# Performance work log

Hardware: AMD Instinct MI355X
Metric: run time of the kernel (lower is better)

## Reference

```python
import jax, jax.numpy as jnp
import numpy as np

B, N, IN_C, HEAD_C, H, EXPAND, OUT_C = 4, 2048, 256, 32, 8, 1024, 256
QKV_DIM = HEAD_C * H * 2 + IN_C * H  # 2560
LN_EPS = 1e-5


def setup_inputs() -> dict:
    key = jax.random.key(0)
    ks = jax.random.split(key, 6)
    s = lambda fan: 1.0 / np.sqrt(fan)
    return {
        "x": jax.random.normal(ks[0], (B, N, IN_C), jnp.float32),
        "ln1_g": jnp.ones((IN_C,), jnp.float32),
        "ln1_b": jnp.zeros((IN_C,), jnp.float32),
        "Wqkv": jax.random.normal(ks[1], (IN_C, QKV_DIM), jnp.float32) * s(IN_C),
        "bqkv": jnp.zeros((QKV_DIM,), jnp.float32),
        "Wm": jax.random.normal(ks[2], (IN_C * H, IN_C), jnp.float32) * s(IN_C * H),
        "bm": jnp.zeros((IN_C,), jnp.float32),
        "ln2_g": jnp.ones((IN_C,), jnp.float32),
        "ln2_b": jnp.zeros((IN_C,), jnp.float32),
        "W1": jax.random.normal(ks[3], (IN_C, EXPAND), jnp.float32) * s(IN_C),
        "b1": jnp.zeros((EXPAND,), jnp.float32),
        "W2": jax.random.normal(ks[4], (EXPAND, OUT_C), jnp.float32) * s(EXPAND),
        "b2": jnp.zeros((OUT_C,), jnp.float32),
    }


def _ln(x, g, b):
    m = x.mean(-1, keepdims=True)
    v = jnp.mean(jnp.square(x - m), axis=-1, keepdims=True)
    return (x - m) * jax.lax.rsqrt(v + LN_EPS) * g + b


def reference(x, ln1_g, ln1_b, Wqkv, bqkv, Wm, bm, ln2_g, ln2_b, W1, b1, W2, b2):
    scale = HEAD_C ** -0.5
    qkv = _ln(x, ln1_g, ln1_b) @ Wqkv + bqkv  # [B,N,QKV_DIM]
    q, k, v = jnp.split(qkv, [HEAD_C * H, 2 * HEAD_C * H], axis=-1)
    q = q.reshape(B, N, H, HEAD_C)  # H-major channel split, matches einops
    k = k.reshape(B, N, H, HEAD_C)
    v = v.reshape(B, N, H, IN_C)    # NOTE: V has in_c channels per head
    attn = jax.nn.softmax(jnp.einsum('bnhc,bmhc->bhnm', q, k) * scale, axis=-1)
    out = jnp.einsum('bhnm,bmhc->bnhc', attn, v).reshape(B, N, H * IN_C)
    x = x + out @ Wm + bm  # residual + merge-head projection
    h = jax.nn.gelu(_ln(x, ln2_g, ln2_b) @ W1 + b1, approximate=False)
    return (h @ W2 + b2) + x  # shortcut is Identity (in_c == out_c)
```

## Files before the change

### kernel.cpp

```cpp
#include <hip/hip_runtime.h>

typedef unsigned short u16;
typedef __attribute__((ext_vector_type(8))) short bf8_t;
typedef __attribute__((ext_vector_type(4))) float f4_t;
typedef __attribute__((ext_vector_type(16))) float fx16;

__device__ __forceinline__ float bf2f(u16 v) {
    union { unsigned u; float f; } c; c.u = ((unsigned)v) << 16; return c.f;
}
__device__ __forceinline__ u16 f2bf(float f) {
    union { float f; unsigned u; } c; c.f = f;
    unsigned r = 0x7FFFu + ((c.u >> 16) & 1u);
    return (u16)((c.u + r) >> 16);
}

#define B_   4
#define N_   2048
#define INC  256
#define H_   8
#define ROWS 8192

#define SEG_X     0
#define SEG_LN1G  2097152
#define SEG_LN1B  2097408
#define SEG_WQKV  2097664
#define SEG_BQKV  2753024
#define SEG_WM    2755584
#define SEG_BM    3279872
#define SEG_LN2G  3280128
#define SEG_LN2B  3280384
#define SEG_W1    3280640
#define SEG_B1    3542784
#define SEG_W2    3543808
#define SEG_B2    3805952
#define SEG_TOT   3806208

__global__ __launch_bounds__(256) void conv_k(
    const void* p0, const void* p1, const void* p2, const void* p3, const void* p4,
    const void* p5, const void* p6, const void* p7, const void* p8, const void* p9,
    const void* p10, const void* p11, const void* p12,
    u16* __restrict__ dst, u16* __restrict__ y, int* __restrict__ mkz)
{
    const int t = threadIdx.x;
    const int blk = blockIdx.x;

    __shared__ int sflag;
    if (t == 0) sflag = 0;
    __syncthreads();
    int bad = 0;
    #pragma unroll
    for (int k2 = 0; k2 < 4; ++k2) {
        float v = bf2f(((const u16*)p0)[t * 4 + k2]);
        if (!(fabsf(v) < 1e10f)) bad = 1;
    }
    if (bad) atomicOr(&sflag, 1);
    __syncthreads();
    const int flag = sflag;

    if (blk == 8192 && t < 32) mkz[t] = 0;

    const int i = blk * 256 + t;
    if (i >= SEG_TOT) return;

    if (i < SEG_LN1G) {
        float v = flag ? ((const float*)p0)[i] : bf2f(((const u16*)p0)[i]);
        dst[i] = f2bf(v);
        float s = v, s2 = v * v;
        #pragma unroll
        for (int d = 1; d < 64; d <<= 1) {
            s  += __shfl_xor(s,  d, 64);
            s2 += __shfl_xor(s2, d, 64);
        }
        __shared__ float rs[8];
        int w = t >> 6;
        if ((t & 63) == 0) { rs[w] = s; rs[4 + w] = s2; }
        __syncthreads();
        s  = rs[0] + rs[1] + rs[2] + rs[3];
        s2 = rs[4] + rs[5] + rs[6] + rs[7];
        float mean = s * (1.0f / INC);
        float var  = s2 * (1.0f / INC) - mean * mean;
        float inv  = rsqrtf(var + 1e-5f);
        float g  = flag ? ((const float*)p1)[t] : bf2f(((const u16*)p1)[t]);
        float bb = flag ? ((const float*)p2)[t] : bf2f(((const u16*)p2)[t]);
        y[i] = f2bf((v - mean) * inv * g + bb);
        return;
    }

    const void* p; int j;
    if      (i < SEG_LN1B) { p = p1;  j = i - SEG_LN1G; }
    else if (i < SEG_WQKV) { p = p2;  j = i - SEG_LN1B; }
    else if (i < SEG_BQKV) { p = p3;  int ii = i - SEG_WQKV;
                             int n = ii >> 8, k = ii & 255; j = k * 2560 + n; }
    else if (i < SEG_WM)   { p = p4;  j = i - SEG_BQKV; }
    else if (i < SEG_BM)   { p = p5;  int ii = i - SEG_WM;
                             int n = ii >> 11, k = ii & 2047; j = k * 256 + n; }
    else if (i < SEG_LN2G) { p = p6;  j = i - SEG_BM; }
    else if (i < SEG_LN2B) { p = p7;  j = i - SEG_LN2G; }
    else if (i < SEG_W1)   { p = p8;  j = i - SEG_LN2B; }
    else if (i < SEG_B1)   { p = p9;  int ii = i - SEG_W1;
                             int n = ii >> 8, k = ii & 255; j = k * 1024 + n; }
    else if (i < SEG_W2)   { p = p10; j = i - SEG_B1; }
    else if (i < SEG_B2)   { p = p11; int ii = i - SEG_W2;
                             int n = ii >> 10, k = ii & 1023; j = k * 256 + n; }
    else                   { p = p12; j = i - SEG_B2; }
    dst[i] = flag ? f2bf(((const float*)p)[j]) : ((const u16*)p)[j];
}

template<bool BF16IN>
__global__ __launch_bounds__(256) void ln_k(const void* __restrict__ xp,
        const u16* __restrict__ g, const u16* __restrict__ b, u16* __restrict__ y)
{
    int row  = blockIdx.x * 4 + (threadIdx.x >> 6);
    int lane = threadIdx.x & 63;
    int c0   = lane * 4;
    float v[4];
    if (BF16IN) {
        ushort4 u = *(const ushort4*)((const u16*)xp + (size_t)row * INC + c0);
        v[0] = bf2f(u.x); v[1] = bf2f(u.y); v[2] = bf2f(u.z); v[3] = bf2f(u.w);
    } else {
        float4 f = *(const float4*)((const float*)xp + (size_t)row * INC + c0);
        v[0] = f.x; v[1] = f.y; v[2] = f.z; v[3] = f.w;
    }
    float s = v[0] + v[1] + v[2] + v[3];
    float s2 = v[0]*v[0] + v[1]*v[1] + v[2]*v[2] + v[3]*v[3];
    #pragma unroll
    for (int d = 1; d < 64; d <<= 1) {
        s  += __shfl_xor(s,  d, 64);
        s2 += __shfl_xor(s2, d, 64);
    }
    float mean = s * (1.0f / INC);
    float var  = s2 * (1.0f / INC) - mean * mean;
    float inv  = rsqrtf(var + 1e-5f);
    ushort4 gv = *(const ushort4*)(g + c0);
    ushort4 bv = *(const ushort4*)(b + c0);
    ushort4 o;
    o.x = f2bf((v[0] - mean) * inv * bf2f(gv.x) + bf2f(bv.x));
    o.y = f2bf((v[1] - mean) * inv * bf2f(gv.y) + bf2f(bv.y));
    o.z = f2bf((v[2] - mean) * inv * bf2f(gv.z) + bf2f(bv.z));
    o.w = f2bf((v[3] - mean) * inv * bf2f(gv.w) + bf2f(bv.w));
    *(ushort4*)(y + (size_t)row * INC + c0) = o;
}

enum { EP_QKV = 0, EP_MERGE = 1, EP_GELU = 2, EP_FFN2 = 3 };

template<int MODE>
__global__ __launch_bounds__(256) void gemm_big(
    const u16* __restrict__ A, const u16* __restrict__ Bt,
    const u16* __restrict__ bias, void* __restrict__ outp,
    u16* __restrict__ qh, u16* __restrict__ kh, u16* __restrict__ vh,
    int* __restrict__ mkz, int N, int K)
{
    const int t = threadIdx.x;
    const int w = t >> 6, lane = t & 63;
    const int l15 = lane & 15, quad = lane >> 4;
    const int col0 = blockIdx.x * 64;
    const int row0 = blockIdx.y * 256;
    const int mrow = row0 + w * 64;

    const u16* Ap = A  + (size_t)(mrow + l15) * K + quad * 8;
    const u16* Bp = Bt + (size_t)(col0 + l15) * K + quad * 8;

    f4_t acc[4][4];
    #pragma unroll
    for (int mi = 0; mi < 4; ++mi)
        #pragma unroll
        for (int ni = 0; ni < 4; ++ni)
            acc[mi][ni] = (f4_t){0.f, 0.f, 0.f, 0.f};

    for (int k0 = 0; k0 < K; k0 += 32) {
        bf8_t a[4], bb[4];
        #pragma unroll
        for (int mi = 0; mi < 4; ++mi)
            a[mi] = *(const bf8_t*)(Ap + (size_t)mi * 16 * K + k0);
        #pragma unroll
        for (int ni = 0; ni < 4; ++ni)
            bb[ni] = *(const bf8_t*)(Bp + (size_t)ni * 16 * K + k0);
        #pragma unroll
        for (int ni = 0; ni < 4; ++ni)
            #pragma unroll
            for (int mi = 0; mi < 4; ++mi)
                acc[mi][ni] = __builtin_amdgcn_mfma_f32_16x16x32_bf16(
                    a[mi], bb[ni], acc[mi][ni], 0, 0, 0);
    }

    if (MODE == EP_QKV) {
        if (col0 >= 512) {
            __shared__ u16 Ts[64][268];
            #pragma unroll
            for (int mi = 0; mi < 4; ++mi)
                #pragma unroll
                for (int ni = 0; ni < 4; ++ni) {
                    float bz = bf2f(bias[col0 + ni * 16 + l15]);
                    #pragma unroll
                    for (int r = 0; r < 4; ++r)
                        Ts[ni * 16 + l15][w * 64 + mi * 16 + quad * 4 + r] =
                            f2bf(acc[mi][ni][r] + bz);
                }
            __syncthreads();
            int vcg = col0 - 512;
            int hh  = vcg >> 8;
            int bb2 = row0 >> 11, nb = row0 & 2047;
            int bhh = bb2 * 8 + hh;
            int tok4 = t & 3, cl = (t >> 2) & 63;
            int vc = (vcg & 255) + cl;
            #pragma unroll
            for (int kb = 0; kb < 16; ++kb) {
                u16* dp = vh + (((size_t)bhh * 128 + ((nb >> 4) + kb)) * 256 + vc) * 16 + tok4 * 4;
                *(ushort4*)dp = *(const ushort4*)&Ts[cl][kb * 16 + tok4 * 4];
            }
        } else if (col0 < 256) {
            #pragma unroll
            for (int mi = 0; mi < 4; ++mi)
                #pragma unroll
                for (int r = 0; r < 4; ++r) {
                    int rg = mrow + mi * 16 + quad * 4 + r;
                    int bb2 = rg >> 11, n = rg & 2047;
                    #pragma unroll
                    for (int ni = 0; ni < 4; ++ni) {
                        int col = col0 + ni * 16 + l15;
                        float v = acc[mi][ni][r] + bf2f(bias[col]);
                        qh[(((size_t)(bb2 * 8 + (col >> 5))) * 2048 + n) * 32 + (col & 31)] = f2bf(v);
                    }
                }
        } else {
            const int hA  = (col0 - 256) >> 5;
            const int bb2 = row0 >> 11;
            float mxA = 0.f, mxB = 0.f;
            #pragma unroll
            for (int mi = 0; mi < 4; ++mi)
                #pragma unroll
                for (int r = 0; r < 4; ++r) {
                    int rg = mrow + mi * 16 + quad * 4 + r;
                    int n = rg & 2047;
                    float vv[4];
                    #pragma unroll
                    for (int ni = 0; ni < 4; ++ni) {
                        int col = col0 + ni * 16 + l15;
                        float v = acc[mi][ni][r] + bf2f(bias[col]);
                        vv[ni] = v;
                        int c2 = col - 256;
                        int hd = c2 >> 5, ch = c2 & 31;
                        kh[(((size_t)(bb2 * 8 + hd) * 64 + (n >> 5)) * 2 + (ch >> 4)) * 512
                           + (n & 31) * 16 + (ch & 15)] = f2bf(v);
                    }
                    float sA = vv[0] * vv[0] + vv[1] * vv[1];
                    float sB = vv[2] * vv[2] + vv[3] * vv[3];
                    #pragma unroll
                    for (int d = 1; d < 16; d <<= 1) {
                        sA += __shfl_xor(sA, d, 64);
                        sB += __shfl_xor(sB, d, 64);
                    }
                    mxA = fmaxf(mxA, sA);
                    mxB = fmaxf(mxB, sB);
                }
            if ((lane & 15) == 0) {
                atomicMax(mkz + bb2 * 8 + hA,     __float_as_int(mxA));
                atomicMax(mkz + bb2 * 8 + hA + 1, __float_as_int(mxB));
            }
        }
    } else {
        float bz[4];
        #pragma unroll
        for (int ni = 0; ni < 4; ++ni) bz[ni] = bf2f(bias[col0 + ni * 16 + l15]);
        #pragma unroll
        for (int mi = 0; mi < 4; ++mi)
            #pragma unroll
            for (int r = 0; r < 4; ++r) {
                int rg = mrow + mi * 16 + quad * 4 + r;
                size_t base = (size_t)rg * N + col0 + l15;
                #pragma unroll
                for (int ni = 0; ni < 4; ++ni) {
                    float v = acc[mi][ni][r] + bz[ni];
                    v = 0.5f * v * (1.0f + erff(v * 0.70710678118654752f));
                    ((u16*)outp)[base + ni * 16] = f2bf(v);
                }
            }
    }
}

template<int MODE>
__global__ __launch_bounds__(256) void gemm_mfma(
    const u16* __restrict__ A, const u16* __restrict__ Bt,
    const u16* __restrict__ bias, const void* __restrict__ res,
    void* __restrict__ outp, int N, int K)
{
    const int t = threadIdx.x;
    const int w = t >> 6, lane = t & 63;
    const int l15 = lane & 15, quad = lane >> 4;
    const int col0 = blockIdx.x * 64;
    const int row0 = blockIdx.y * 128;
    const int mrow = row0 + w * 32;

    const u16* Ap = A  + (size_t)(mrow + l15) * K + quad * 8;
    const u16* Bp = Bt + (size_t)(col0 + l15) * K + quad * 8;

    f4_t acc[2][4];
    #pragma unroll
    for (int mi = 0; mi < 2; ++mi)
        #pragma unroll
        for (int ni = 0; ni < 4; ++ni)
            acc[mi][ni] = (f4_t){0.f, 0.f, 0.f, 0.f};

    for (int k0 = 0; k0 < K; k0 += 64) {
        bf8_t a[2][2], bb[4][2];
        #pragma unroll
        for (int kc = 0; kc < 2; ++kc) {
            #pragma unroll
            for (int mi = 0; mi < 2; ++mi)
                a[mi][kc] = *(const bf8_t*)(Ap + (size_t)mi * 16 * K + k0 + kc * 32);
            #pragma unroll
            for (int ni = 0; ni < 4; ++ni)
                bb[ni][kc] = *(const bf8_t*)(Bp + (size_t)ni * 16 * K + k0 + kc * 32);
        }
        #pragma unroll
        for (int kc = 0; kc < 2; ++kc)
            #pragma unroll
            for (int ni = 0; ni < 4; ++ni)
                #pragma unroll
                for (int mi = 0; mi < 2; ++mi)
                    acc[mi][ni] = __builtin_amdgcn_mfma_f32_16x16x32_bf16(
                        a[mi][kc], bb[ni][kc], acc[mi][ni], 0, 0, 0);
    }

    float bz[4];
    #pragma unroll
    for (int ni = 0; ni < 4; ++ni) bz[ni] = bf2f(bias[col0 + ni * 16 + l15]);
    #pragma unroll
    for (int mi = 0; mi < 2; ++mi)
        #pragma unroll
        for (int r = 0; r < 4; ++r) {
            int rg = mrow + mi * 16 + quad * 4 + r;
            size_t base = (size_t)rg * N + col0 + l15;
            if (MODE == EP_MERGE) {
                const u16* R = (const u16*)res;
                #pragma unroll
                for (int ni = 0; ni < 4; ++ni)
                    ((float*)outp)[base + ni * 16] =
                        acc[mi][ni][r] + bz[ni] + bf2f(R[base + ni * 16]);
            } else {
                const float* R = (const float*)res;
                #pragma unroll
                for (int ni = 0; ni < 4; ++ni)
                    ((float*)outp)[base + ni * 16] =
                        acc[mi][ni][r] + bz[ni] + R[base + ni * 16];
            }
        }
}

__global__ __launch_bounds__(256) void attn_k(
    const u16* __restrict__ qh, const u16* __restrict__ kh,
    const u16* __restrict__ vhT, const float* __restrict__ mk2,
    u16* __restrict__ ao)
{
    const int t = threadIdx.x;
    const int w = t >> 6, lane = t & 63;
    const int l31 = lane & 31, hi = lane >> 5;
    const int id = blockIdx.x;
    const int qt = (id >> 3) & 31;
    const int bh = (id >> 8) * 8 + (id & 7);
    const int b  = bh >> 3, h = bh & 7;
    const int n0 = qt * 64;
    const float SCALE = 0.17677669529663687f;
    const int sw = (l31 & 7) << 4;

    __shared__ __align__(16) u16 Pb[2][64][128];
    __shared__ float lds_l[4][64];
    __shared__ float lds_t[64];

    bf8_t qf[2][2];
    #pragma unroll
    for (int m = 0; m < 2; ++m)
        #pragma unroll
        for (int ks = 0; ks < 2; ++ks)
            qf[m][ks] = *(const bf8_t*)(qh + ((size_t)bh * 2048 + n0 + m * 32 + l31) * 32
                                        + ks * 16 + hi * 8);

    float mrow[2];
    #pragma unroll
    for (int m = 0; m < 2; ++m) {
        float q2 = 0.f;
        #pragma unroll
        for (int ks = 0; ks < 2; ++ks)
            #pragma unroll
            for (int i = 0; i < 8; ++i) {
                float qv = bf2f((u16)qf[m][ks][i]); q2 += qv * qv;
            }
        q2 += __shfl_xor(q2, 32, 64);
        mrow[m] = SCALE * sqrtf(q2 * mk2[bh]);
    }

    fx16 acc[2][2];
    #pragma unroll
    for (int a1 = 0; a1 < 2; ++a1)
        #pragma unroll
        for (int a2 = 0; a2 < 2; ++a2)
            #pragma unroll
            for (int e = 0; e < 16; ++e) acc[a1][a2][e] = 0.f;
    float lsum[2] = {0.f, 0.f};

    fx16 z16;
    #pragma unroll
    for (int e = 0; e < 16; ++e) z16[e] = 0.f;

    auto finish = [&](const fx16& s, int m, int g, char* base) {
        float p0 = __expf(fmaf(s[4 * g + 0], SCALE, -mrow[m]));
        float p1 = __expf(fmaf(s[4 * g + 1], SCALE, -mrow[m]));
        float p2 = __expf(fmaf(s[4 * g + 2], SCALE, -mrow[m]));
        float p3 = __expf(fmaf(s[4 * g + 3], SCALE, -mrow[m]));
        lsum[m] += (p0 + p1) + (p2 + p3);
        ushort4 pk;
        pk.x = f2bf(p0); pk.y = f2bf(p1); pk.z = f2bf(p2); pk.w = f2bf(p3);
        *(ushort4*)(base + (m * 32 + l31) * 256 + ((w * 64 + 16 * g + 8 * hi) ^ sw)) = pk;
    };

    bf8_t kA0, kA1;
    auto ldK = [&](int c) {
        const u16* kp = kh + ((size_t)bh * 64 + c * 4 + w) * 1024 + l31 * 16 + hi * 8;
        kA0 = *(const bf8_t*)kp;
        kA1 = *(const bf8_t*)(kp + 512);
    };

    {
        ldK(0);
        fx16 sA = __builtin_amdgcn_mfma_f32_32x32x16_bf16(kA0, qf[0][0], z16, 0, 0, 0);
        sA = __builtin_amdgcn_mfma_f32_32x32x16_bf16(kA1, qf[0][1], sA, 0, 0, 0);
        fx16 sB = __builtin_amdgcn_mfma_f32_32x32x16_bf16(kA0, qf[1][0], z16, 0, 0, 0);
        sB = __builtin_amdgcn_mfma_f32_32x32x16_bf16(kA1, qf[1][1], sB, 0, 0, 0);
        ldK(1);
        char* base0 = (char*)&Pb[0][0][0];
        #pragma unroll
        for (int g = 0; g < 4; ++g) finish(sA, 0, g, base0);
        #pragma unroll
        for (int g = 0; g < 4; ++g) finish(sB, 1, g, base0);
    }

    const u16* vpb = vhT + (((size_t)bh * 128) * 256 + w * 64 + l31) * 16 + hi * 8;
    bf8_t vb0 = *(const bf8_t*)vpb;
    bf8_t vb1 = *(const bf8_t*)(vpb + 512);

    int buf = 0;
    for (int c = 0; c < 16; ++c, buf ^= 1) {
        __syncthreads();
        const bool qn = (c < 15);
        fx16 sA, sB;
        if (qn) {
            sA = __builtin_amdgcn_mfma_f32_32x32x16_bf16(kA0, qf[0][0], z16, 0, 0, 0);
            sA = __builtin_amdgcn_mfma_f32_32x32x16_bf16(kA1, qf[0][1], sA, 0, 0, 0);
        }
        const char* pb = (const char*)&Pb[buf][0][0];
        char* wr = (char*)&Pb[buf ^ 1][0][0];
        const u16* vp = vpb + (size_t)c * 32768;
        #pragma unroll
        for (int ks = 0; ks < 8; ++ks) {
            bf8_t nv0 = *(const bf8_t*)(vp + (ks + 1) * 4096);
            bf8_t nv1 = *(const bf8_t*)(vp + (ks + 1) * 4096 + 512);
            bf8_t pa0 = *(const bf8_t*)(pb + l31 * 256        + ((ks * 32 + hi * 16) ^ sw));
            bf8_t pa1 = *(const bf8_t*)(pb + (32 + l31) * 256 + ((ks * 32 + hi * 16) ^ sw));
            __builtin_amdgcn_s_setprio(1);
            acc[0][0] = __builtin_amdgcn_mfma_f32_32x32x16_bf16(pa0, vb0, acc[0][0], 0, 0, 0);
            acc[0][1] = __builtin_amdgcn_mfma_f32_32x32x16_bf16(pa0, vb1, acc[0][1], 0, 0, 0);
            acc[1][0] = __builtin_amdgcn_mfma_f32_32x32x16_bf16(pa1, vb0, acc[1][0], 0, 0, 0);
            acc[1][1] = __builtin_amdgcn_mfma_f32_32x32x16_bf16(pa1, vb1, acc[1][1], 0, 0, 0);
            __builtin_amdgcn_s_setprio(0);
            if (qn) {
                if (ks < 4) {
                    finish(sA, 0, ks, wr);
                    if (ks == 3) {
                        sB = __builtin_amdgcn_mfma_f32_32x32x16_bf16(kA0, qf[1][0], z16, 0, 0, 0);
                        sB = __builtin_amdgcn_mfma_f32_32x32x16_bf16(kA1, qf[1][1], sB, 0, 0, 0);
                        if (c < 14) ldK(c + 2);
                    }
                } else {
                    finish(sB, 1, ks - 4, wr);
                }
            }
            vb0 = nv0; vb1 = nv1;
        }
    }

    #pragma unroll
    for (int m = 0; m < 2; ++m) {
        lsum[m] += __shfl_xor(lsum[m], 32, 64);
        if (hi == 0) lds_l[w][m * 32 + l31] = lsum[m];
    }
    __syncthreads();
    if (t < 64) lds_t[t] = lds_l[0][t] + lds_l[1][t] + lds_l[2][t] + lds_l[3][t];
    __syncthreads();

    #pragma unroll
    for (int mt = 0; mt < 2; ++mt)
        #pragma unroll
        for (int g = 0; g < 4; ++g) {
            f4_t lv = *(const f4_t*)&lds_t[mt * 32 + 8 * g + 4 * hi];
            #pragma unroll
            for (int j = 0; j < 4; ++j) {
                float inv = 1.0f / lv[j];
                int q = mt * 32 + 8 * g + 4 * hi + j;
                size_t rowbase = ((size_t)(b * 2048 + n0 + q)) * 2048 + h * 256 + w * 64;
                #pragma unroll
                for (int nt = 0; nt < 2; ++nt)
                    ao[rowbase + nt * 32 + l31] = f2bf(acc[mt][nt][g * 4 + j] * inv);
            }
        }
}

extern "C" void kernel_launch(void* const* d_in, const int* in_sizes, int n_in,
                              void* d_out, int out_size, void* d_ws, size_t ws_size,
                              hipStream_t stream)
{
    u16* wsu = (u16*)d_ws;
    float* mk = (float*)(wsu + 64);

    const size_t CVT0 = 128;
    const size_t Y0   = CVT0 + SEG_TOT;
    const size_t QH0  = Y0  + 2097152;
    const size_t KH0  = QH0 + 2097152;
    const size_t VT0  = KH0 + 2097152;
    const size_t AO0  = VT0 + 16777216;
    const size_t X20  = AO0 + 16777216;

    u16* cvt = wsu + CVT0;
    u16* y   = wsu + Y0;
    u16* qh  = wsu + QH0;
    u16* kh  = wsu + KH0;
    u16* vhT = wsu + VT0;
    u16* ao  = wsu + AO0;
    float* x2 = (float*)(wsu + X20);
    u16* hbb  = wsu + AO0;

    const u16* xc   = cvt + SEG_X;
    const u16* Wqkv = cvt + SEG_WQKV;
    const u16* bqkv = cvt + SEG_BQKV;
    const u16* Wm   = cvt + SEG_WM;
    const u16* bm   = cvt + SEG_BM;
    const u16* ln2g = cvt + SEG_LN2G;
    const u16* ln2b = cvt + SEG_LN2B;
    const u16* W1   = cvt + SEG_W1;
    const u16* b1   = cvt + SEG_B1;
    const u16* W2   = cvt + SEG_W2;
    const u16* b2   = cvt + SEG_B2;

    conv_k<<<SEG_TOT / 256, 256, 0, stream>>>(
        d_in[0], d_in[1], d_in[2], d_in[3], d_in[4], d_in[5], d_in[6],
        d_in[7], d_in[8], d_in[9], d_in[10], d_in[11], d_in[12],
        cvt, y, (int*)mk);

    gemm_big<EP_QKV><<<dim3(2560 / 64, ROWS / 256), 256, 0, stream>>>(
        y, Wqkv, bqkv, nullptr, qh, kh, vhT, (int*)mk, 2560, 256);
    attn_k<<<1024, 256, 0, stream>>>(qh, kh, vhT, mk, ao);
    gemm_mfma<EP_MERGE><<<dim3(256 / 64, ROWS / 128), 256, 0, stream>>>(
        ao, Wm, bm, xc, x2, 256, 2048);
    ln_k<false><<<ROWS / 4, 256, 0, stream>>>(x2, ln2g, ln2b, y);
    gemm_big<EP_GELU><<<dim3(1024 / 64, ROWS / 256), 256, 0, stream>>>(
        y, W1, b1, hbb, nullptr, nullptr, nullptr, nullptr, 1024, 256);
    gemm_mfma<EP_FFN2><<<dim3(256 / 64, ROWS / 128), 256, 0, stream>>>(
        hbb, W2, b2, x2, d_out, 256, 1024);
}
```

Measured before the change: 337.7 us.

## Transpose weights via LDS tiles and shrink skinny GEMM row tiles

Weight transposes move out of the elementwise conversion kernel into a dedicated kernel that stages 64x64 tiles in LDS. This gives coalesced reads and writes instead of strided global reads. The skinny N=256 GEMMs now use 64-row blocks with one M-fragment per wave, doubling the block count to improve occupancy and CU coverage. The trade-off is an extra kernel launch and less reuse of B loads per block.

```diff
diff --git a/kernel.cpp b/kernel.cpp
--- a/kernel.cpp
+++ b/kernel.cpp
@@ -35,34 +35,67 @@
 #define SEG_B2    3805952
 #define SEG_TOT   3806208
 
+__device__ __forceinline__ int sniff_flag(const void* x0, int t, int* sh) {
+    if (t == 0) *sh = 0;
+    __syncthreads();
+    int bad = 0;
+    #pragma unroll
+    for (int k2 = 0; k2 < 4; ++k2) {
+        float v = bf2f(((const u16*)x0)[t * 4 + k2]);
+        if (!(fabsf(v) < 1e10f)) bad = 1;
+    }
+    if (bad) atomicOr(sh, 1);
+    __syncthreads();
+    return *sh;
+}
+
+__global__ __launch_bounds__(256) void trans_k(
+    const void* x0, const void* pWqkv, const void* pWm, const void* pW1, const void* pW2,
+    u16* __restrict__ dst)
+{
+    const int t = threadIdx.x;
+    __shared__ int sflag;
+    const int flag = sniff_flag(x0, t, &sflag);
+
+    const int blk = blockIdx.x;
+    const void* W; int Kd, Nd, kt, nt; size_t seg;
+    if (blk < 160)      { W = pWqkv; Kd = 256;  Nd = 2560; kt = blk / 40;  nt = blk % 40;  seg = SEG_WQKV; }
+    else if (blk < 288) { int i2 = blk - 160; W = pWm; Kd = 2048; Nd = 256;  kt = i2 >> 2;  nt = i2 & 3;  seg = SEG_WM; }
+    else if (blk < 352) { int i2 = blk - 288; W = pW1; Kd = 256;  Nd = 1024; kt = i2 >> 4;  nt = i2 & 15; seg = SEG_W1; }
+    else                { int i2 = blk - 352; W = pW2; Kd = 1024; Nd = 256;  kt = i2 >> 2;  nt = i2 & 3;  seg = SEG_W2; }
+    const int k0 = kt * 64, n0 = nt * 64;
+
+    __shared__ u16 Tl[64][66];
+    #pragma unroll
+    for (int p = 0; p < 16; ++p) {
+        int idx = t + p * 256;
+        int r = idx >> 6, c = idx & 63;
+        size_t si = (size_t)(k0 + r) * Nd + n0 + c;
+        Tl[r][c] = flag ? f2bf(((const float*)W)[si]) : ((const u16*)W)[si];
+    }
+    __syncthreads();
+    u16* dp = dst + seg;
+    #pragma unroll
+    for (int p = 0; p < 8; ++p) {
+        int idx = t + p * 256;
+        int rn = idx >> 5, ck = (idx & 31) * 2;
+        ushort2 v; v.x = Tl[ck][rn]; v.y = Tl[ck + 1][rn];
+        *(ushort2*)(dp + (size_t)(n0 + rn) * Kd + k0 + ck) = v;
+    }
+}
+
 __global__ __launch_bounds__(256) void conv_k(
-    const void* p0, const void* p1, const void* p2, const void* p3, const void* p4,
-    const void* p5, const void* p6, const void* p7, const void* p8, const void* p9,
-    const void* p10, const void* p11, const void* p12,
+    const void* p0, const void* p1, const void* p2, const void* p4, const void* p6,
+    const void* p7, const void* p8, const void* p10, const void* p12,
     u16* __restrict__ dst, u16* __restrict__ y, int* __restrict__ mkz)
 {
     const int t = threadIdx.x;
     const int blk = blockIdx.x;
-
     __shared__ int sflag;
-    if (t == 0) sflag = 0;
-    __syncthreads();
-    int bad = 0;
-    #pragma unroll
-    for (int k2 = 0; k2 < 4; ++k2) {
-        float v = bf2f(((const u16*)p0)[t * 4 + k2]);
-        if (!(fabsf(v) < 1e10f)) bad = 1;
-    }
-    if (bad) atomicOr(&sflag, 1);
-    __syncthreads();
-    const int flag = sflag;
-
-    if (blk == 8192 && t < 32) mkz[t] = 0;
-
-    const int i = blk * 256 + t;
-    if (i >= SEG_TOT) return;
-
-    if (i < SEG_LN1G) {
+    const int flag = sniff_flag(p0, t, &sflag);
+
+    if (blk < 8192) {
+        const int i = blk * 256 + t;
         float v = flag ? ((const float*)p0)[i] : bf2f(((const u16*)p0)[i]);
         dst[i] = f2bf(v);
         float s = v, s2 = v * v;
@@ -86,24 +119,17 @@
         return;
     }
 
-    const void* p; int j;
-    if      (i < SEG_LN1B) { p = p1;  j = i - SEG_LN1G; }
-    else if (i < SEG_WQKV) { p = p2;  j = i - SEG_LN1B; }
-    else if (i < SEG_BQKV) { p = p3;  int ii = i - SEG_WQKV;
-                             int n = ii >> 8, k = ii & 255; j = k * 2560 + n; }
-    else if (i < SEG_WM)   { p = p4;  j = i - SEG_BQKV; }
-    else if (i < SEG_BM)   { p = p5;  int ii = i - SEG_WM;
-                             int n = ii >> 11, k = ii & 2047; j = k * 256 + n; }
-    else if (i < SEG_LN2G) { p = p6;  j = i - SEG_BM; }
-    else if (i < SEG_LN2B) { p = p7;  j = i - SEG_LN2G; }
-    else if (i < SEG_W1)   { p = p8;  j = i - SEG_LN2B; }
-    else if (i < SEG_B1)   { p = p9;  int ii = i - SEG_W1;
-                             int n = ii >> 8, k = ii & 255; j = k * 1024 + n; }
-    else if (i < SEG_W2)   { p = p10; j = i - SEG_B1; }
-    else if (i < SEG_B2)   { p = p11; int ii = i - SEG_W2;
-                             int n = ii >> 10, k = ii & 1023; j = k * 256 + n; }
-    else                   { p = p12; j = i - SEG_B2; }
-    dst[i] = flag ? f2bf(((const float*)p)[j]) : ((const u16*)p)[j];
+    if (blk == 8192 && t < 32) mkz[t] = 0;
+
+    const int elem = (blk - 8192) * 256 + t;
+    const void* p; int j; size_t doff;
+    if      (elem < 2560) { p = p4;  j = elem;        doff = SEG_BQKV + j; }
+    else if (elem < 2816) { p = p6;  j = elem - 2560; doff = SEG_BM   + j; }
+    else if (elem < 3072) { p = p7;  j = elem - 2816; doff = SEG_LN2G + j; }
+    else if (elem < 3328) { p = p8;  j = elem - 3072; doff = SEG_LN2B + j; }
+    else if (elem < 4352) { p = p10; j = elem - 3328; doff = SEG_B1   + j; }
+    else                  { p = p12; j = elem - 4352; doff = SEG_B2   + j; }
+    dst[doff] = flag ? f2bf(((const float*)p)[j]) : ((const u16*)p)[j];
 }
 
 template<bool BF16IN>
@@ -288,26 +314,22 @@
     const int w = t >> 6, lane = t & 63;
     const int l15 = lane & 15, quad = lane >> 4;
     const int col0 = blockIdx.x * 64;
-    const int row0 = blockIdx.y * 128;
-    const int mrow = row0 + w * 32;
+    const int row0 = blockIdx.y * 64;
+    const int mrow = row0 + w * 16;
 
     const u16* Ap = A  + (size_t)(mrow + l15) * K + quad * 8;
     const u16* Bp = Bt + (size_t)(col0 + l15) * K + quad * 8;
 
-    f4_t acc[2][4];
-    #pragma unroll
-    for (int mi = 0; mi < 2; ++mi)
-        #pragma unroll
-        for (int ni = 0; ni < 4; ++ni)
-            acc[mi][ni] = (f4_t){0.f, 0.f, 0.f, 0.f};
+    f4_t acc[4];
+    #pragma unroll
+    for (int ni = 0; ni < 4; ++ni)
+        acc[ni] = (f4_t){0.f, 0.f, 0.f, 0.f};
 
     for (int k0 = 0; k0 < K; k0 += 64) {
-        bf8_t a[2][2], bb[4][2];
+        bf8_t a[2], bb[4][2];
         #pragma unroll
         for (int kc = 0; kc < 2; ++kc) {
-            #pragma unroll
-            for (int mi = 0; mi < 2; ++mi)
-                a[mi][kc] = *(const bf8_t*)(Ap + (size_t)mi * 16 * K + k0 + kc * 32);
+            a[kc] = *(const bf8_t*)(Ap + k0 + kc * 32);
             #pragma unroll
             for (int ni = 0; ni < 4; ++ni)
                 bb[ni][kc] = *(const bf8_t*)(Bp + (size_t)ni * 16 * K + k0 + kc * 32);
@@ -316,35 +338,31 @@
         for (int kc = 0; kc < 2; ++kc)
             #pragma unroll
             for (int ni = 0; ni < 4; ++ni)
-                #pragma unroll
-                for (int mi = 0; mi < 2; ++mi)
-                    acc[mi][ni] = __builtin_amdgcn_mfma_f32_16x16x32_bf16(
-                        a[mi][kc], bb[ni][kc], acc[mi][ni], 0, 0, 0);
+                acc[ni] = __builtin_amdgcn_mfma_f32_16x16x32_bf16(
+                    a[kc], bb[ni][kc], acc[ni], 0, 0, 0);
     }
 
     float bz[4];
     #pragma unroll
     for (int ni = 0; ni < 4; ++ni) bz[ni] = bf2f(bias[col0 + ni * 16 + l15]);
     #pragma unroll
-    for (int mi = 0; mi < 2; ++mi)
-        #pragma unroll
-        for (int r = 0; r < 4; ++r) {
-            int rg = mrow + mi * 16 + quad * 4 + r;
-            size_t base = (size_t)rg * N + col0 + l15;
-            if (MODE == EP_MERGE) {
-                const u16* R = (const u16*)res;
-                #pragma unroll
-                for (int ni = 0; ni < 4; ++ni)
-                    ((float*)outp)[base + ni * 16] =
-                        acc[mi][ni][r] + bz[ni] + bf2f(R[base + ni * 16]);
-            } else {
-                const float* R = (const float*)res;
-                #pragma unroll
-                for (int ni = 0; ni < 4; ++ni)
-                    ((float*)outp)[base + ni * 16] =
-                        acc[mi][ni][r] + bz[ni] + R[base + ni * 16];
-            }
-        }
+    for (int r = 0; r < 4; ++r) {
+        int rg = mrow + quad * 4 + r;
+        size_t base = (size_t)rg * N + col0 + l15;
+        if (MODE == EP_MERGE) {
+            const u16* R = (const u16*)res;
+            #pragma unroll
+            for (int ni = 0; ni < 4; ++ni)
+                ((float*)outp)[base + ni * 16] =
+                    acc[ni][r] + bz[ni] + bf2f(R[base + ni * 16]);
+        } else {
+            const float* R = (const float*)res;
+            #pragma unroll
+            for (int ni = 0; ni < 4; ++ni)
+                ((float*)outp)[base + ni * 16] =
+                    acc[ni][r] + bz[ni] + R[base + ni * 16];
+        }
+    }
 }
 
 __global__ __launch_bounds__(256) void attn_k(
@@ -540,19 +558,20 @@
     const u16* W2   = cvt + SEG_W2;
     const u16* b2   = cvt + SEG_B2;
 
-    conv_k<<<SEG_TOT / 256, 256, 0, stream>>>(
-        d_in[0], d_in[1], d_in[2], d_in[3], d_in[4], d_in[5], d_in[6],
-        d_in[7], d_in[8], d_in[9], d_in[10], d_in[11], d_in[12],
-        cvt, y, (int*)mk);
+    conv_k<<<8192 + 18, 256, 0, stream>>>(
+        d_in[0], d_in[1], d_in[2], d_in[4], d_in[6], d_in[7], d_in[8],
+        d_in[10], d_in[12], cvt, y, (int*)mk);
+    trans_k<<<416, 256, 0, stream>>>(
+        d_in[0], d_in[3], d_in[5], d_in[9], d_in[11], cvt);
 
     gemm_big<EP_QKV><<<dim3(2560 / 64, ROWS / 256), 256, 0, stream>>>(
         y, Wqkv, bqkv, nullptr, qh, kh, vhT, (int*)mk, 2560, 256);
     attn_k<<<1024, 256, 0, stream>>>(qh, kh, vhT, mk, ao);
-    gemm_mfma<EP_MERGE><<<dim3(256 / 64, ROWS / 128), 256, 0, stream>>>(
+    gemm_mfma<EP_MERGE><<<dim3(256 / 64, ROWS / 64), 256, 0, stream>>>(
         ao, Wm, bm, xc, x2, 256, 2048);
     ln_k<false><<<ROWS / 4, 256, 0, stream>>>(x2, ln2g, ln2b, y);
     gemm_big<EP_GELU><<<dim3(1024 / 64, ROWS / 256), 256, 0, stream>>>(
         y, W1, b1, hbb, nullptr, nullptr, nullptr, nullptr, 1024, 256);
-    gemm_mfma<EP_FFN2><<<dim3(256 / 64, ROWS / 128), 256, 0, stream>>>(
+    gemm_mfma<EP_FFN2><<<dim3(256 / 64, ROWS / 64), 256, 0, stream>>>(
         hbb, W2, b2, x2, d_out, 256, 1024);
 }
```

Measured after the change: 379.2 us. +12.3%, slower.
